# Kernel tuning notes

Measured on AMD Instinct MI355X. Metric: run time of the kernel, lower is better.

The kernel has to match this reference:

```python
import jax, jax.numpy as jnp
import numpy as np

B, N, D = 4, 2048, 1024
H = 16
HD = D // H  # head_dim = 64
SCALE = HD ** -0.5


def setup_inputs() -> dict:
    key = jax.random.key(0)
    k1, k2, k3, k4 = jax.random.split(key, 4)
    x = jax.random.normal(k1, (B, N, D), dtype=jnp.float32)
    # init-scale weights for numerically sane softmax logits
    w_qkv = jax.random.normal(k2, (3 * D, D), dtype=jnp.float32) * 0.02
    w_proj = jax.random.normal(k3, (D, D), dtype=jnp.float32) * 0.02
    b_proj = jax.random.normal(k4, (D,), dtype=jnp.float32) * 0.02
    return {"x": x, "w_qkv": w_qkv, "w_proj": w_proj, "b_proj": b_proj}


def reference(x, w_qkv, w_proj, b_proj):
    # qkv projection (width_mult=1.0 -> Dyna slicing is identity; qkv_bias=False)
    qkv = jnp.einsum('bnd,ed->bne', x, w_qkv)          # (B, N, 3D)
    qkv = qkv.reshape(B, N, 3, H, HD)
    q = qkv[:, :, 0].transpose(0, 2, 1, 3)              # (B, H, N, HD)
    k = qkv[:, :, 1].transpose(0, 2, 1, 3)
    v = qkv[:, :, 2].transpose(0, 2, 1, 3)
    q = q * SCALE
    attn = jnp.einsum('bhqd,bhkd->bhqk', q, k)          # (B, H, N, N)
    attn = jax.nn.softmax(attn, axis=-1)
    out = jnp.einsum('bhqk,bhkd->bhqd', attn, v)        # (B, H, N, HD)
    out = out.transpose(0, 2, 1, 3).reshape(B, N, D)
    # output projection (bias=True)
    return jnp.einsum('bnd,ed->bne', out, w_proj) + b_proj
```

## Files before the change

### kernel.cpp

```cpp
#include <hip/hip_runtime.h>
#include <hip/hip_bf16.h>
#include <stdint.h>


typedef __attribute__((ext_vector_type(8))) short short8;
typedef __attribute__((ext_vector_type(4))) short short4v;
typedef __attribute__((ext_vector_type(4))) float float4v;

#define MFMA16(a, b, c) __builtin_amdgcn_mfma_f32_16x16x32_bf16((a), (b), (c), 0, 0, 0)

static __device__ __forceinline__ unsigned short f2bf(float f) {
  union { float f; unsigned u; } v; v.f = f;
  unsigned r = v.u + 0x7fffu + ((v.u >> 16) & 1u);
  return (unsigned short)(r >> 16);
}
static __device__ __forceinline__ float bf2f(unsigned short u) {
  union { unsigned u; float f; } v; v.u = ((unsigned)u) << 16;
  return v.f;
}
static __device__ __forceinline__ unsigned pkbf(float a, float b) {
  union { __hip_bfloat162 v; unsigned u; } c;
  c.v = __float22bfloat162_rn(make_float2(a, b));
  return c.u;
}
static __device__ __forceinline__ float4v fzero() {
  float4v z; z[0] = 0.f; z[1] = 0.f; z[2] = 0.f; z[3] = 0.f; return z;
}
static __device__ __forceinline__ void load_lds16(const void* g, void* l) {
  typedef const __attribute__((address_space(1))) void* gp_t;
  typedef __attribute__((address_space(3))) void* lp_t;
  __builtin_amdgcn_global_load_lds((gp_t)(uintptr_t)g, (lp_t)(uint32_t)(uintptr_t)l, 16, 0, 0);
}

__global__ void detect_dtype(const unsigned short* __restrict__ x, int* flag) {
  __shared__ int cnt;
  if (threadIdx.x == 0) cnt = 0;
  __syncthreads();
  int c = 0;
  for (int i = threadIdx.x; i < 4096; i += 256) {
    const unsigned v = x[i] & 0x7FFFu;
    if ((v >> 7) >= 134u) ++c;
  }
  atomicAdd(&cnt, c);
  __syncthreads();
  if (threadIdx.x == 0) *flag = (cnt > 64) ? 1 : 0;
}

static __device__ __forceinline__ void cv8(const void* src, unsigned short* dst,
                                           int i, int fl) {
  if (fl) {
    const float* s = (const float*)src + i;
    short8 o;
    for (int j = 0; j < 8; ++j) o[j] = (short)f2bf(s[j]);
    *(short8*)(dst + i) = o;
  } else {
    *(short8*)(dst + i) = *(const short8*)((const unsigned short*)src + i);
  }
}
__global__ __launch_bounds__(256) void convert_all(
    const void* __restrict__ s0, const void* __restrict__ s1,
    const void* __restrict__ s2, const void* __restrict__ s3,
    unsigned short* __restrict__ d0, unsigned short* __restrict__ d1,
    unsigned short* __restrict__ d2, unsigned short* __restrict__ d3,
    const int* __restrict__ flag) {
  const int t = blockIdx.x * 256 + threadIdx.x;
  const int fl = *flag;
  if (t < 1048576)       cv8(s0, d0, t * 8, fl);
  else if (t < 1441792)  cv8(s1, d1, (t - 1048576) * 8, fl);
  else if (t < 1572864)  cv8(s2, d2, (t - 1441792) * 8, fl);
  else if (t < 1572992)  cv8(s3, d3, (t - 1572864) * 8, fl);
}

__global__ __launch_bounds__(256) void qkv_gemm(
    const unsigned short* __restrict__ X, const unsigned short* __restrict__ W,
    unsigned short* __restrict__ Qo, unsigned short* __restrict__ Ko,
    unsigned short* __restrict__ Vt) {
  __shared__ __attribute__((aligned(16))) unsigned short lA[128 * 32];
  __shared__ __attribute__((aligned(16))) unsigned short lB[128 * 32];
  const int tid = threadIdx.x;
  const int wave = tid >> 6, lane = tid & 63, quad = lane >> 4, l16 = lane & 15;
  const int wm = wave >> 1, wn = wave & 1;
  const int m0 = blockIdx.x * 128, n0 = blockIdx.y * 128;

  float4v acc[4][4];
  for (int i = 0; i < 4; ++i) for (int j = 0; j < 4; ++j) acc[i][j] = fzero();

  const int f0 = tid, f1 = 256 + tid;
  const int r0 = f0 >> 2, c0 = (f0 & 3) * 8;
  const int r1 = f1 >> 2, c1 = (f1 & 3) * 8;
  unsigned short* dA0 = lA + (wave * 64) * 8;
  unsigned short* dA1 = lA + (256 + wave * 64) * 8;
  unsigned short* dB0 = lB + (wave * 64) * 8;
  unsigned short* dB1 = lB + (256 + wave * 64) * 8;

  for (int k0 = 0; k0 < 1024; k0 += 32) {
    __syncthreads();
    load_lds16(X + (size_t)(m0 + r0) * 1024 + k0 + c0, dA0);
    load_lds16(X + (size_t)(m0 + r1) * 1024 + k0 + c1, dA1);
    load_lds16(W + (size_t)(n0 + r0) * 1024 + k0 + c0, dB0);
    load_lds16(W + (size_t)(n0 + r1) * 1024 + k0 + c1, dB1);
    __syncthreads();
    short8 af[4], bfr[4];
    for (int t = 0; t < 4; ++t) {
      af[t]  = *(const short8*)(lA + (wm * 64 + t * 16 + l16) * 32 + quad * 8);
      bfr[t] = *(const short8*)(lB + (wn * 64 + t * 16 + l16) * 32 + quad * 8);
    }
    for (int mt = 0; mt < 4; ++mt)
      for (int nt = 0; nt < 4; ++nt)
        acc[mt][nt] = MFMA16(af[mt], bfr[nt], acc[mt][nt]);
  }

  for (int mt = 0; mt < 4; ++mt) {
    const int mbase = m0 + wm * 64 + mt * 16 + quad * 4;
    const int b = mbase >> 11;
    const int nrow = mbase & 2047;
    for (int nt = 0; nt < 4; ++nt) {
      const int e = n0 + wn * 64 + nt * 16 + l16;
      const int c = e >> 10, h = (e >> 6) & 15, hd = e & 63;
      const int bh = b * 16 + h;
      if (c == 0) {
        for (int r = 0; r < 4; ++r)
          Qo[((size_t)bh * 2048 + nrow + r) * 64 + hd] = f2bf(acc[mt][nt][r] * 0.125f);
      } else if (c == 1) {
        for (int r = 0; r < 4; ++r)
          Ko[((size_t)bh * 2048 + nrow + r) * 64 + hd] = f2bf(acc[mt][nt][r]);
      } else {
        short4v pk;
        for (int r = 0; r < 4; ++r) pk[r] = (short)f2bf(acc[mt][nt][r]);
        *(short4v*)(Vt + ((size_t)bh * 64 + hd) * 2048 + nrow) = pk;
      }
    }
  }
}

__global__ __launch_bounds__(256, 2) void flash_attn(
    const unsigned short* __restrict__ Q, const unsigned short* __restrict__ K,
    const unsigned short* __restrict__ Vt, unsigned short* __restrict__ AO) {
  __shared__ __attribute__((aligned(16))) unsigned short lK[64 * 72];
  __shared__ __attribute__((aligned(16))) unsigned short lV[64 * 72];
  __shared__ __attribute__((aligned(16))) unsigned short lP[4][32 * 72];
  const int tid = threadIdx.x;
  const int wave = tid >> 6, lane = tid & 63, quad = lane >> 4, l16 = lane & 15;
  const int qt = blockIdx.x, bh = blockIdx.y;
  const int b = bh >> 4, h = bh & 15;
  const size_t base = (size_t)bh * 2048 * 64;
  const unsigned short* Qp = Q + base;
  const unsigned short* Kp = K + base;
  const unsigned short* Vp = Vt + base;
  const int q0 = qt * 128;

  const int qa = q0 + wave * 16 + l16;
  const short8 qfA0 = *(const short8*)(Qp + (size_t)qa * 64 + quad * 8);
  const short8 qfA1 = *(const short8*)(Qp + (size_t)qa * 64 + 32 + quad * 8);
  const short8 qfB0 = *(const short8*)(Qp + (size_t)(qa + 64) * 64 + quad * 8);
  const short8 qfB1 = *(const short8*)(Qp + (size_t)(qa + 64) * 64 + 32 + quad * 8);

  float4v oaccA[4], oaccB[4];
  for (int i = 0; i < 4; ++i) { oaccA[i] = fzero(); oaccB[i] = fzero(); }
  float lsumA[4] = {0.f, 0.f, 0.f, 0.f};
  float lsumB[4] = {0.f, 0.f, 0.f, 0.f};
  unsigned short* myP = lP[wave];

  const int f0 = tid, f1 = 256 + tid;
  const int sk0 = (f0 >> 3) * 72 + (f0 & 7) * 8;
  const int sk1 = (f1 >> 3) * 72 + (f1 & 7) * 8;

  for (int kb = 0; kb < 32; ++kb) {
    const short8 kv0 = *(const short8*)(Kp + (size_t)kb * 4096 + f0 * 8);
    const short8 kv1 = *(const short8*)(Kp + (size_t)kb * 4096 + f1 * 8);
    const short8 vv0 = *(const short8*)(Vp + (size_t)(f0 >> 3) * 2048 + kb * 64 + (f0 & 7) * 8);
    const short8 vv1 = *(const short8*)(Vp + (size_t)(f1 >> 3) * 2048 + kb * 64 + (f1 & 7) * 8);
    __syncthreads();
    *(short8*)(lK + sk0) = kv0;
    *(short8*)(lK + sk1) = kv1;
    *(short8*)(lV + sk0) = vv0;
    *(short8*)(lV + sk1) = vv1;
    __syncthreads();

    float4v sA[4], sB[4];
    for (int t = 0; t < 4; ++t) {
      const short8 k0f = *(const short8*)(lK + (t * 16 + l16) * 72 + quad * 8);
      const short8 k1f = *(const short8*)(lK + (t * 16 + l16) * 72 + 32 + quad * 8);
      sA[t] = MFMA16(qfA0, k0f, fzero());
      sA[t] = MFMA16(qfA1, k1f, sA[t]);
      sB[t] = MFMA16(qfB0, k0f, fzero());
      sB[t] = MFMA16(qfB1, k1f, sB[t]);
    }

    for (int t = 0; t < 4; ++t)
      for (int r = 0; r < 4; ++r) {
        const float pA = __expf(sA[t][r]);
        const float pB = __expf(sB[t][r]);
        sA[t][r] = pA; lsumA[r] += pA;
        sB[t][r] = pB; lsumB[r] += pB;
      }

    for (int r = 0; r < 4; ++r) {
      const int rowA = (quad * 4 + r) * 72;
      const int rowB = rowA + 16 * 72;
      const unsigned a01 = pkbf(sA[0][r], sA[1][r]);
      const unsigned a23 = pkbf(sA[2][r], sA[3][r]);
      const unsigned b01 = pkbf(sB[0][r], sB[1][r]);
      const unsigned b23 = pkbf(sB[2][r], sB[3][r]);
      myP[rowA + l16]      = (unsigned short)a01;
      myP[rowA + 16 + l16] = (unsigned short)(a01 >> 16);
      myP[rowA + 32 + l16] = (unsigned short)a23;
      myP[rowA + 48 + l16] = (unsigned short)(a23 >> 16);
      myP[rowB + l16]      = (unsigned short)b01;
      myP[rowB + 16 + l16] = (unsigned short)(b01 >> 16);
      myP[rowB + 32 + l16] = (unsigned short)b23;
      myP[rowB + 48 + l16] = (unsigned short)(b23 >> 16);
    }
    asm volatile("s_waitcnt lgkmcnt(0)" ::: "memory");
    const short8 paA0 = *(const short8*)(myP + l16 * 72 + quad * 8);
    const short8 paA1 = *(const short8*)(myP + l16 * 72 + 32 + quad * 8);
    const short8 paB0 = *(const short8*)(myP + (16 + l16) * 72 + quad * 8);
    const short8 paB1 = *(const short8*)(myP + (16 + l16) * 72 + 32 + quad * 8);

    for (int nt = 0; nt < 4; ++nt) {
      const short8 v0 = *(const short8*)(lV + (nt * 16 + l16) * 72 + quad * 8);
      const short8 v1 = *(const short8*)(lV + (nt * 16 + l16) * 72 + 32 + quad * 8);
      oaccA[nt] = MFMA16(paA0, v0, oaccA[nt]);
      oaccA[nt] = MFMA16(paA1, v1, oaccA[nt]);
      oaccB[nt] = MFMA16(paB0, v0, oaccB[nt]);
      oaccB[nt] = MFMA16(paB1, v1, oaccB[nt]);
    }
  }

  for (int r = 0; r < 4; ++r) {
    lsumA[r] += __shfl_xor(lsumA[r], 1);
    lsumA[r] += __shfl_xor(lsumA[r], 2);
    lsumA[r] += __shfl_xor(lsumA[r], 4);
    lsumA[r] += __shfl_xor(lsumA[r], 8);
    lsumB[r] += __shfl_xor(lsumB[r], 1);
    lsumB[r] += __shfl_xor(lsumB[r], 2);
    lsumB[r] += __shfl_xor(lsumB[r], 4);
    lsumB[r] += __shfl_xor(lsumB[r], 8);
  }

  for (int r = 0; r < 4; ++r) {
    const float invA = 1.f / lsumA[r];
    const float invB = 1.f / lsumB[r];
    const int nA = q0 + wave * 16 + quad * 4 + r;
    for (int nt = 0; nt < 4; ++nt) {
      AO[((size_t)(b * 2048 + nA)) * 1024 + h * 64 + nt * 16 + l16] =
          f2bf(oaccA[nt][r] * invA);
      AO[((size_t)(b * 2048 + nA + 64)) * 1024 + h * 64 + nt * 16 + l16] =
          f2bf(oaccB[nt][r] * invB);
    }
  }
}

__global__ __launch_bounds__(256) void proj_gemm(
    const unsigned short* __restrict__ A, const unsigned short* __restrict__ W,
    const unsigned short* __restrict__ bias_bf, const void* __restrict__ bias_raw,
    void* __restrict__ outv, const int* __restrict__ flag) {
  __shared__ __attribute__((aligned(16))) unsigned short lA[128 * 32];
  __shared__ __attribute__((aligned(16))) unsigned short lB[128 * 32];
  const int tid = threadIdx.x;
  const int wave = tid >> 6, lane = tid & 63, quad = lane >> 4, l16 = lane & 15;
  const int wm = wave >> 1, wn = wave & 1;
  const int m0 = blockIdx.x * 128, n0 = blockIdx.y * 128;
  const int fl = *flag;

  float4v acc[4][4];
  for (int i = 0; i < 4; ++i) for (int j = 0; j < 4; ++j) acc[i][j] = fzero();

  const int f0 = tid, f1 = 256 + tid;
  const int r0 = f0 >> 2, c0 = (f0 & 3) * 8;
  const int r1 = f1 >> 2, c1 = (f1 & 3) * 8;
  unsigned short* dA0 = lA + (wave * 64) * 8;
  unsigned short* dA1 = lA + (256 + wave * 64) * 8;
  unsigned short* dB0 = lB + (wave * 64) * 8;
  unsigned short* dB1 = lB + (256 + wave * 64) * 8;

  for (int k0 = 0; k0 < 1024; k0 += 32) {
    __syncthreads();
    load_lds16(A + (size_t)(m0 + r0) * 1024 + k0 + c0, dA0);
    load_lds16(A + (size_t)(m0 + r1) * 1024 + k0 + c1, dA1);
    load_lds16(W + (size_t)(n0 + r0) * 1024 + k0 + c0, dB0);
    load_lds16(W + (size_t)(n0 + r1) * 1024 + k0 + c1, dB1);
    __syncthreads();
    short8 af[4], bfr[4];
    for (int t = 0; t < 4; ++t) {
      af[t]  = *(const short8*)(lA + (wm * 64 + t * 16 + l16) * 32 + quad * 8);
      bfr[t] = *(const short8*)(lB + (wn * 64 + t * 16 + l16) * 32 + quad * 8);
    }
    for (int mt = 0; mt < 4; ++mt)
      for (int nt = 0; nt < 4; ++nt)
        acc[mt][nt] = MFMA16(af[mt], bfr[nt], acc[mt][nt]);
  }

  for (int mt = 0; mt < 4; ++mt) {
    const int mbase = m0 + wm * 64 + mt * 16 + quad * 4;
    for (int nt = 0; nt < 4; ++nt) {
      const int e = n0 + wn * 64 + nt * 16 + l16;
      const float bv = fl ? ((const float*)bias_raw)[e] : bf2f(bias_bf[e]);
      for (int r = 0; r < 4; ++r) {
        const float val = acc[mt][nt][r] + bv;
        const size_t idx = (size_t)(mbase + r) * 1024 + e;
        if (fl) ((float*)outv)[idx] = val;
        else    ((unsigned short*)outv)[idx] = f2bf(val);
      }
    }
  }
}

extern "C" void kernel_launch(void* const* d_in, const int* in_sizes, int n_in,
                              void* d_out, int out_size, void* d_ws, size_t ws_size,
                              hipStream_t stream) {
  const void* x_raw     = d_in[0];
  const void* wqkv_raw  = d_in[1];
  const void* wproj_raw = d_in[2];
  const void* bproj_raw = d_in[3];

  const size_t NE = (size_t)4 * 16 * 2048 * 64;
  unsigned short* ws = (unsigned short*)d_ws;
  unsigned short* Q      = ws;
  unsigned short* K      = Q + NE;
  unsigned short* Vt     = K + NE;
  unsigned short* xb     = Vt + NE;
  unsigned short* AO     = xb;
  unsigned short* wqkvb  = xb + NE;
  unsigned short* wprojb = wqkvb + 3145728;
  unsigned short* bprojb = wprojb + 1048576;
  int* flag = (int*)(bprojb + 1024);

  detect_dtype<<<1, 256, 0, stream>>>((const unsigned short*)x_raw, flag);
  convert_all<<<6145, 256, 0, stream>>>(x_raw, wqkv_raw, wproj_raw, bproj_raw,
                                        xb, wqkvb, wprojb, bprojb, flag);

  qkv_gemm<<<dim3(64, 24), 256, 0, stream>>>(xb, wqkvb, Q, K, Vt);
  flash_attn<<<dim3(16, 64), 256, 0, stream>>>(Q, K, Vt, AO);
  proj_gemm<<<dim3(64, 8), 256, 0, stream>>>(AO, wprojb, bprojb, bproj_raw,
                                             d_out, flag);
}
```

Measured before the change: 299.0 us.

## Keep softmax probabilities in registers via transposed QK^T MFMA layout

Computes S transposed (K as the A operand), so each lane's exp'd score fragment already matches the B-operand layout of a 16x16x16 MFMA for the PV product. This removes the per-wave LDS round trip for P, along with its LDS stores, wait and reloads. Row sums shrink to one scalar per lane and output stores become packed 4-wide. The launch-bound occupancy hint rises from 2 to 4 blocks now that the P buffer no longer uses LDS, at the cost of twice as many K=16 MFMAs and register pressure under the tighter bound.

```diff
diff --git a/kernel.cpp b/kernel.cpp
--- a/kernel.cpp
+++ b/kernel.cpp
@@ -8,6 +8,7 @@
 typedef __attribute__((ext_vector_type(4))) float float4v;
 
 #define MFMA16(a, b, c) __builtin_amdgcn_mfma_f32_16x16x32_bf16((a), (b), (c), 0, 0, 0)
+#define MFMA16K16(a, b, c) __builtin_amdgcn_mfma_f32_16x16x16bf16_1k((a), (b), (c), 0, 0, 0)
 
 static __device__ __forceinline__ unsigned short f2bf(float f) {
   union { float f; unsigned u; } v; v.f = f;
@@ -133,12 +134,11 @@
   }
 }
 
-__global__ __launch_bounds__(256, 2) void flash_attn(
+__global__ __launch_bounds__(256, 4) void flash_attn(
     const unsigned short* __restrict__ Q, const unsigned short* __restrict__ K,
     const unsigned short* __restrict__ Vt, unsigned short* __restrict__ AO) {
   __shared__ __attribute__((aligned(16))) unsigned short lK[64 * 72];
   __shared__ __attribute__((aligned(16))) unsigned short lV[64 * 72];
-  __shared__ __attribute__((aligned(16))) unsigned short lP[4][32 * 72];
   const int tid = threadIdx.x;
   const int wave = tid >> 6, lane = tid & 63, quad = lane >> 4, l16 = lane & 15;
   const int qt = blockIdx.x, bh = blockIdx.y;
@@ -157,9 +157,7 @@
 
   float4v oaccA[4], oaccB[4];
   for (int i = 0; i < 4; ++i) { oaccA[i] = fzero(); oaccB[i] = fzero(); }
-  float lsumA[4] = {0.f, 0.f, 0.f, 0.f};
-  float lsumB[4] = {0.f, 0.f, 0.f, 0.f};
-  unsigned short* myP = lP[wave];
+  float lsumA = 0.f, lsumB = 0.f;
 
   const int f0 = tid, f1 = 256 + tid;
   const int sk0 = (f0 >> 3) * 72 + (f0 & 7) * 8;
@@ -181,73 +179,50 @@
     for (int t = 0; t < 4; ++t) {
       const short8 k0f = *(const short8*)(lK + (t * 16 + l16) * 72 + quad * 8);
       const short8 k1f = *(const short8*)(lK + (t * 16 + l16) * 72 + 32 + quad * 8);
-      sA[t] = MFMA16(qfA0, k0f, fzero());
-      sA[t] = MFMA16(qfA1, k1f, sA[t]);
-      sB[t] = MFMA16(qfB0, k0f, fzero());
-      sB[t] = MFMA16(qfB1, k1f, sB[t]);
-    }
-
-    for (int t = 0; t < 4; ++t)
-      for (int r = 0; r < 4; ++r) {
-        const float pA = __expf(sA[t][r]);
-        const float pB = __expf(sB[t][r]);
-        sA[t][r] = pA; lsumA[r] += pA;
-        sB[t][r] = pB; lsumB[r] += pB;
+      sA[t] = MFMA16(k0f, qfA0, fzero());
+      sA[t] = MFMA16(k1f, qfA1, sA[t]);
+      sB[t] = MFMA16(k0f, qfB0, fzero());
+      sB[t] = MFMA16(k1f, qfB1, sB[t]);
+    }
+
+    short4v pA[4], pB[4];
+    for (int t = 0; t < 4; ++t) {
+      float eA0 = __expf(sA[t][0]), eA1 = __expf(sA[t][1]);
+      float eA2 = __expf(sA[t][2]), eA3 = __expf(sA[t][3]);
+      float eB0 = __expf(sB[t][0]), eB1 = __expf(sB[t][1]);
+      float eB2 = __expf(sB[t][2]), eB3 = __expf(sB[t][3]);
+      lsumA += (eA0 + eA1) + (eA2 + eA3);
+      lsumB += (eB0 + eB1) + (eB2 + eB3);
+      union { unsigned u[2]; short4v s; } ca, cb;
+      ca.u[0] = pkbf(eA0, eA1); ca.u[1] = pkbf(eA2, eA3);
+      cb.u[0] = pkbf(eB0, eB1); cb.u[1] = pkbf(eB2, eB3);
+      pA[t] = ca.s; pB[t] = cb.s;
+    }
+
+    for (int nt = 0; nt < 4; ++nt) {
+      const unsigned short* vrow = lV + (nt * 16 + l16) * 72 + quad * 4;
+      for (int t = 0; t < 4; ++t) {
+        const short4v vf = *(const short4v*)(vrow + t * 16);
+        oaccA[nt] = MFMA16K16(vf, pA[t], oaccA[nt]);
+        oaccB[nt] = MFMA16K16(vf, pB[t], oaccB[nt]);
       }
-
-    for (int r = 0; r < 4; ++r) {
-      const int rowA = (quad * 4 + r) * 72;
-      const int rowB = rowA + 16 * 72;
-      const unsigned a01 = pkbf(sA[0][r], sA[1][r]);
-      const unsigned a23 = pkbf(sA[2][r], sA[3][r]);
-      const unsigned b01 = pkbf(sB[0][r], sB[1][r]);
-      const unsigned b23 = pkbf(sB[2][r], sB[3][r]);
-      myP[rowA + l16]      = (unsigned short)a01;
-      myP[rowA + 16 + l16] = (unsigned short)(a01 >> 16);
-      myP[rowA + 32 + l16] = (unsigned short)a23;
-      myP[rowA + 48 + l16] = (unsigned short)(a23 >> 16);
-      myP[rowB + l16]      = (unsigned short)b01;
-      myP[rowB + 16 + l16] = (unsigned short)(b01 >> 16);
-      myP[rowB + 32 + l16] = (unsigned short)b23;
-      myP[rowB + 48 + l16] = (unsigned short)(b23 >> 16);
-    }
-    asm volatile("s_waitcnt lgkmcnt(0)" ::: "memory");
-    const short8 paA0 = *(const short8*)(myP + l16 * 72 + quad * 8);
-    const short8 paA1 = *(const short8*)(myP + l16 * 72 + 32 + quad * 8);
-    const short8 paB0 = *(const short8*)(myP + (16 + l16) * 72 + quad * 8);
-    const short8 paB1 = *(const short8*)(myP + (16 + l16) * 72 + 32 + quad * 8);
-
-    for (int nt = 0; nt < 4; ++nt) {
-      const short8 v0 = *(const short8*)(lV + (nt * 16 + l16) * 72 + quad * 8);
-      const short8 v1 = *(const short8*)(lV + (nt * 16 + l16) * 72 + 32 + quad * 8);
-      oaccA[nt] = MFMA16(paA0, v0, oaccA[nt]);
-      oaccA[nt] = MFMA16(paA1, v1, oaccA[nt]);
-      oaccB[nt] = MFMA16(paB0, v0, oaccB[nt]);
-      oaccB[nt] = MFMA16(paB1, v1, oaccB[nt]);
-    }
-  }
-
-  for (int r = 0; r < 4; ++r) {
-    lsumA[r] += __shfl_xor(lsumA[r], 1);
-    lsumA[r] += __shfl_xor(lsumA[r], 2);
-    lsumA[r] += __shfl_xor(lsumA[r], 4);
-    lsumA[r] += __shfl_xor(lsumA[r], 8);
-    lsumB[r] += __shfl_xor(lsumB[r], 1);
-    lsumB[r] += __shfl_xor(lsumB[r], 2);
-    lsumB[r] += __shfl_xor(lsumB[r], 4);
-    lsumB[r] += __shfl_xor(lsumB[r], 8);
-  }
-
-  for (int r = 0; r < 4; ++r) {
-    const float invA = 1.f / lsumA[r];
-    const float invB = 1.f / lsumB[r];
-    const int nA = q0 + wave * 16 + quad * 4 + r;
-    for (int nt = 0; nt < 4; ++nt) {
-      AO[((size_t)(b * 2048 + nA)) * 1024 + h * 64 + nt * 16 + l16] =
-          f2bf(oaccA[nt][r] * invA);
-      AO[((size_t)(b * 2048 + nA + 64)) * 1024 + h * 64 + nt * 16 + l16] =
-          f2bf(oaccB[nt][r] * invB);
-    }
+    }
+  }
+
+  lsumA += __shfl_xor(lsumA, 16); lsumA += __shfl_xor(lsumA, 32);
+  lsumB += __shfl_xor(lsumB, 16); lsumB += __shfl_xor(lsumB, 32);
+  const float invA = 1.f / lsumA, invB = 1.f / lsumB;
+
+  unsigned short* aoA = AO + ((size_t)(b * 2048 + qa)) * 1024 + h * 64 + quad * 4;
+  unsigned short* aoB = aoA + (size_t)64 * 1024;
+  for (int nt = 0; nt < 4; ++nt) {
+    union { unsigned u[2]; short4v s; } oa, ob;
+    oa.u[0] = pkbf(oaccA[nt][0] * invA, oaccA[nt][1] * invA);
+    oa.u[1] = pkbf(oaccA[nt][2] * invA, oaccA[nt][3] * invA);
+    ob.u[0] = pkbf(oaccB[nt][0] * invB, oaccB[nt][1] * invB);
+    ob.u[1] = pkbf(oaccB[nt][2] * invB, oaccB[nt][3] * invB);
+    *(short4v*)(aoA + nt * 16) = oa.s;
+    *(short4v*)(aoB + nt * 16) = ob.s;
   }
 }
 
```

After: 291.2 us. 1.03x faster.
